# Kernel tuning notes

Hardware: AMD Instinct MI355X
Metric: run time of the kernel (lower is better)

The kernel has to match this reference:

```python
import jax, jax.numpy as jnp
import numpy as np

HIDDEN = 64
LATENT = 32
HEADS = 4
EDGE_DIM = 3
NEG_SLOPE = 0.2
N_NODES = 50000
N_EDGES = 400000
IN_DIM = 128
NUM_CLASSES = 10
NUM_GRAPHS = 64


def _gatv2_layer(x, src, dst, edge_attr, Wl, Wr, We, att, b):
    # x: [N, F]; src/dst: [E] (self-loops already included); edge_attr: [E, 3]
    N = x.shape[0]
    xl = (x @ Wl).reshape(N, HEADS, HIDDEN)          # source transform (lin_l)
    xr = (x @ Wr).reshape(N, HEADS, HIDDEN)          # target transform (lin_r)
    e = (edge_attr @ We).reshape(-1, HEADS, HIDDEN)  # edge transform (lin_edge)
    s = jax.nn.leaky_relu(xl[src] + xr[dst] + e, NEG_SLOPE)   # [E,H,C]
    logits = jnp.einsum('ehc,hc->eh', s, att)                 # [E,H]
    # segment softmax over incoming edges of each destination node
    m = jax.ops.segment_max(logits, dst, num_segments=N)      # [N,H]
    ex = jnp.exp(logits - m[dst])
    denom = jax.ops.segment_sum(ex, dst, num_segments=N)      # [N,H]
    alpha = ex / denom[dst]                                   # [E,H]
    msg = xl[src] * alpha[:, :, None]                         # [E,H,C]
    out = jax.ops.segment_sum(msg, dst, num_segments=N)       # [N,H,C]
    return out.mean(axis=1) + b                               # concat=False -> head mean


def setup_inputs() -> dict:
    key = jax.random.key(0)
    ks = jax.random.split(key, 24)
    inp = {}
    inp['x'] = jax.random.normal(ks[0], (N_NODES, IN_DIM), dtype=jnp.float32)
    inp['edge_index'] = jax.random.randint(ks[1], (2, N_EDGES), 0, N_NODES)
    inp['edge_attr'] = jax.random.normal(ks[2], (N_EDGES, EDGE_DIM), dtype=jnp.float32)
    inp['batch'] = jnp.sort(jax.random.randint(ks[3], (N_NODES,), 0, NUM_GRAPHS))
    HC = HEADS * HIDDEN

    def glorot(k, shape):
        fan = shape[0] + shape[-1]
        return jax.random.normal(k, shape, dtype=jnp.float32) * jnp.sqrt(2.0 / fan)

    # layer 0 (in_dim -> hidden), layer 1 (hidden -> hidden)
    inp['Wl0'] = glorot(ks[4], (IN_DIM, HC)); inp['Wr0'] = glorot(ks[5], (IN_DIM, HC))
    inp['We0'] = glorot(ks[6], (EDGE_DIM, HC)); inp['att0'] = glorot(ks[7], (HEADS, HIDDEN))
    inp['b0'] = jnp.zeros((HIDDEN,), jnp.float32)
    inp['Wl1'] = glorot(ks[8], (HIDDEN, HC)); inp['Wr1'] = glorot(ks[9], (HIDDEN, HC))
    inp['We1'] = glorot(ks[10], (EDGE_DIM, HC)); inp['att1'] = glorot(ks[11], (HEADS, HIDDEN))
    inp['b1'] = jnp.zeros((HIDDEN,), jnp.float32)
    inp['W_mu'] = glorot(ks[12], (HIDDEN, LATENT)); inp['b_mu'] = jnp.zeros((LATENT,), jnp.float32)
    inp['W_dec'] = glorot(ks[13], (LATENT, IN_DIM)); inp['b_dec'] = jnp.zeros((IN_DIM,), jnp.float32)
    inp['W_cls'] = glorot(ks[14], (LATENT, NUM_CLASSES)); inp['b_cls'] = jnp.zeros((NUM_CLASSES,), jnp.float32)
    inp['weight'] = jax.random.normal(ks[15], (LATENT,), dtype=jnp.float32)
    return inp


def reference(x, edge_index, edge_attr, batch,
              Wl0, Wr0, We0, att0, b0,
              Wl1, Wr1, We1, att1, b1,
              W_mu, b_mu, W_dec, b_dec, W_cls, b_cls, weight):
    N = x.shape[0]
    # add self-loops once (PyG add_self_loops=True; edge_attr fill_value='mean')
    loops = jnp.arange(N, dtype=edge_index.dtype)
    src = jnp.concatenate([edge_index[0], loops])
    dst = jnp.concatenate([edge_index[1], loops])
    ea_mean = jnp.mean(edge_attr, axis=0)
    ea = jnp.concatenate([edge_attr, jnp.broadcast_to(ea_mean, (N, EDGE_DIM))], axis=0)

    h = jax.nn.relu(_gatv2_layer(x, src, dst, ea, Wl0, Wr0, We0, att0, b0))
    h = jax.nn.relu(_gatv2_layer(h, src, dst, ea, Wl1, Wr1, We1, att1, b1))
    z = h @ W_mu + b_mu                                   # [N, LATENT]

    recon = z @ W_dec + b_dec                             # node_recon: [N, in_dim]
    link = jnp.sum(z[edge_index[0]] * z[edge_index[1]] * weight, axis=1)  # [E]
    g_emb = jax.ops.segment_sum(z, batch, num_segments=NUM_GRAPHS)        # global_add_pool
    logits = g_emb @ W_cls + b_cls                        # [G, num_classes]
    return z, recon, link, logits
```

## Files before the change

kernel.cpp:

```cpp
#include <hip/hip_runtime.h>
#include <math.h>

#define HIDDEN 64
#define LATENT 32
#define HEADS 4
#define IN_DIM 128
#define NUM_CLASSES 10
#define NUM_GRAPHS 64
#define NEG_SLOPE 0.2f
#define HC 256

__global__ void k_easum(const float* __restrict__ ea, int E, float* __restrict__ ea_sum) {
    float s0 = 0.f, s1 = 0.f, s2 = 0.f;
    for (int e = blockIdx.x * blockDim.x + threadIdx.x; e < E; e += gridDim.x * blockDim.x) {
        s0 += ea[e * 3 + 0];
        s1 += ea[e * 3 + 1];
        s2 += ea[e * 3 + 2];
    }
    for (int off = 32; off; off >>= 1) {
        s0 += __shfl_xor(s0, off);
        s1 += __shfl_xor(s1, off);
        s2 += __shfl_xor(s2, off);
    }
    if ((threadIdx.x & 63) == 0) {
        atomicAdd(&ea_sum[0], s0);
        atomicAdd(&ea_sum[1], s1);
        atomicAdd(&ea_sum[2], s2);
    }
}

__global__ void k_hist(const int* __restrict__ ei, int* __restrict__ deg, int E0) {
    int e = blockIdx.x * blockDim.x + threadIdx.x;
    if (e < E0) atomicAdd(&deg[ei[E0 + e]], 1);
}

__global__ void k_scan1(const int* __restrict__ deg, int* __restrict__ off,
                        int* __restrict__ bsum, int N) {
    __shared__ int sh[256];
    int t = threadIdx.x, i = blockIdx.x * 256 + t;
    int v = (i < N) ? deg[i] : 0;
    sh[t] = v;
    __syncthreads();
    for (int d = 1; d < 256; d <<= 1) {
        int x = (t >= d) ? sh[t - d] : 0;
        __syncthreads();
        sh[t] += x;
        __syncthreads();
    }
    if (i < N) off[i] = sh[t] - v;
    if (t == 255) bsum[blockIdx.x] = sh[255];
}

__global__ void k_scan2(int* __restrict__ bsum, int nb) {
    __shared__ int sh[256];
    int t = threadIdx.x;
    int v = (t < nb) ? bsum[t] : 0;
    sh[t] = v;
    __syncthreads();
    for (int d = 1; d < 256; d <<= 1) {
        int x = (t >= d) ? sh[t - d] : 0;
        __syncthreads();
        sh[t] += x;
        __syncthreads();
    }
    if (t < nb) bsum[t] = sh[t] - v;
}

__global__ void k_scan3(int* __restrict__ off, const int* __restrict__ bsum,
                        int* __restrict__ cur, int N) {
    int i = blockIdx.x * 256 + threadIdx.x;
    if (i >= N) return;
    int o = off[i] + bsum[blockIdx.x];
    off[i] = o;
    cur[i] = o;
}

__global__ void k_scatter(const int* __restrict__ ei, const float* __restrict__ ea,
                          int* __restrict__ cur, int* __restrict__ csr_src,
                          float4* __restrict__ csr_a, int E0) {
    int e = blockIdx.x * blockDim.x + threadIdx.x;
    if (e >= E0) return;
    int dst = ei[E0 + e];
    int pos = atomicAdd(&cur[dst], 1);
    csr_src[pos] = ei[e];
    csr_a[pos] = make_float4(ea[e * 3], ea[e * 3 + 1], ea[e * 3 + 2], 0.f);
}

template <int K, int NPB>
__global__ void k_dual_gemm(const float* __restrict__ X, const float* __restrict__ Wl,
                            const float* __restrict__ Wr, float* __restrict__ xl,
                            float* __restrict__ xr, int N) {
    __shared__ float sx[NPB][K];
    int node0 = blockIdx.x * NPB;
    int tid = threadIdx.x;
    for (int i = tid; i < NPB * K; i += blockDim.x) {
        int n = i / K, k = i % K;
        int gn = node0 + n;
        sx[n][k] = (gn < N) ? X[(long)gn * K + k] : 0.f;
    }
    __syncthreads();
    int col = tid;
    float accl[NPB], accr[NPB];
#pragma unroll
    for (int n = 0; n < NPB; n++) { accl[n] = 0.f; accr[n] = 0.f; }
    for (int k = 0; k < K; k++) {
        float wl = Wl[k * HC + col];
        float wr = Wr[k * HC + col];
#pragma unroll
        for (int n = 0; n < NPB; n++) {
            accl[n] += sx[n][k] * wl;
            accr[n] += sx[n][k] * wr;
        }
    }
#pragma unroll
    for (int n = 0; n < NPB; n++) {
        int gn = node0 + n;
        if (gn < N) {
            xl[(long)gn * HC + col] = accl[n];
            xr[(long)gn * HC + col] = accr[n];
        }
    }
}

__global__ void k_gat(const float* __restrict__ xl, const float* __restrict__ xr,
                      const int* __restrict__ csr_src, const float4* __restrict__ csr_a,
                      const int* __restrict__ off, const int* __restrict__ deg,
                      const float* __restrict__ easum, float invE,
                      const float* __restrict__ We, const float* __restrict__ att,
                      const float* __restrict__ bias, float* __restrict__ out, int N) {
    int wid = (blockIdx.x * blockDim.x + threadIdx.x) >> 6;
    int L = threadIdx.x & 63;
    if (wid >= N) return;
    int n = wid;

    float4 xr4 = ((const float4*)(xr + (size_t)n * HC))[L];
    float4 w0 = ((const float4*)We)[L];
    float4 w1 = ((const float4*)(We + HC))[L];
    float4 w2 = ((const float4*)(We + 2 * HC))[L];
    float4 at = ((const float4*)att)[L];
    float am0 = easum[0] * invE, am1 = easum[1] * invE, am2 = easum[2] * invE;

    float m = -INFINITY, d = 0.f;
    float acc0 = 0.f, acc1 = 0.f, acc2 = 0.f, acc3 = 0.f;
    int base = off[n], cnt = deg[n];

    for (int i = -1; i < cnt; i++) {
        int src;
        float a0, a1, a2;
        if (i < 0) {
            src = n;
            a0 = am0; a1 = am1; a2 = am2;
        } else {
            src = csr_src[base + i];
            float4 a = csr_a[base + i];
            a0 = a.x; a1 = a.y; a2 = a.z;
        }
        float4 xs = ((const float4*)(xl + (size_t)src * HC))[L];
        float s0 = xs.x + xr4.x + (a0 * w0.x + a1 * w1.x + a2 * w2.x);
        float s1 = xs.y + xr4.y + (a0 * w0.y + a1 * w1.y + a2 * w2.y);
        float s2 = xs.z + xr4.z + (a0 * w0.z + a1 * w1.z + a2 * w2.z);
        float s3 = xs.w + xr4.w + (a0 * w0.w + a1 * w1.w + a2 * w2.w);
        s0 = (s0 > 0.f) ? s0 : NEG_SLOPE * s0;
        s1 = (s1 > 0.f) ? s1 : NEG_SLOPE * s1;
        s2 = (s2 > 0.f) ? s2 : NEG_SLOPE * s2;
        s3 = (s3 > 0.f) ? s3 : NEG_SLOPE * s3;
        float p = s0 * at.x + s1 * at.y + s2 * at.z + s3 * at.w;
        p += __shfl_xor(p, 1);
        p += __shfl_xor(p, 2);
        p += __shfl_xor(p, 4);
        p += __shfl_xor(p, 8);
        float mn = fmaxf(m, p);
        float sc = __expf(m - mn);
        float ex = __expf(p - mn);
        d = d * sc + ex;
        acc0 = acc0 * sc + ex * xs.x;
        acc1 = acc1 * sc + ex * xs.y;
        acc2 = acc2 * sc + ex * xs.z;
        acc3 = acc3 * sc + ex * xs.w;
        m = mn;
    }
    float inv_d = 1.f / d;
    float v0 = acc0 * inv_d, v1 = acc1 * inv_d, v2 = acc2 * inv_d, v3 = acc3 * inv_d;
    v0 += __shfl_xor(v0, 16); v1 += __shfl_xor(v1, 16);
    v2 += __shfl_xor(v2, 16); v3 += __shfl_xor(v3, 16);
    v0 += __shfl_xor(v0, 32); v1 += __shfl_xor(v1, 32);
    v2 += __shfl_xor(v2, 32); v3 += __shfl_xor(v3, 32);
    if (L < 16) {
        float4 bx = ((const float4*)bias)[L];
        float4 o;
        o.x = fmaxf(0.25f * v0 + bx.x, 0.f);
        o.y = fmaxf(0.25f * v1 + bx.y, 0.f);
        o.z = fmaxf(0.25f * v2 + bx.z, 0.f);
        o.w = fmaxf(0.25f * v3 + bx.w, 0.f);
        ((float4*)(out + (size_t)n * HIDDEN))[L] = o;
    }
}

__global__ void k_mu(const float* __restrict__ h, const float* __restrict__ Wmu,
                     const float* __restrict__ bmu, float* __restrict__ z, int N) {
    int i = blockIdx.x * blockDim.x + threadIdx.x;
    if (i >= N * LATENT) return;
    int n = i >> 5, j = i & 31;
    const float* hr = h + (long)n * 64;
    float acc = bmu[j];
#pragma unroll
    for (int k = 0; k < 64; k++) acc += hr[k] * Wmu[k * LATENT + j];
    z[i] = acc;
}

__global__ void k_dec(const float* __restrict__ z, const float* __restrict__ W,
                      const float* __restrict__ b, float* __restrict__ out, int N) {
    int i = blockIdx.x * blockDim.x + threadIdx.x;
    if (i >= N * IN_DIM) return;
    int n = i >> 7, j = i & 127;
    const float* zr = z + (long)n * LATENT;
    float acc = b[j];
#pragma unroll
    for (int k = 0; k < LATENT; k++) acc += zr[k] * W[k * IN_DIM + j];
    out[i] = acc;
}

__global__ void k_link(const float* __restrict__ z, const int* __restrict__ ei,
                       const float* __restrict__ w, float* __restrict__ link, int E0) {
    int t = blockIdx.x * blockDim.x + threadIdx.x;
    int e = t >> 5;
    int c = t & 31;
    if (e >= E0) return;
    int s = ei[e], d = ei[E0 + e];
    float v = z[(long)s * LATENT + c] * z[(long)d * LATENT + c] * w[c];
    for (int off = 16; off; off >>= 1) v += __shfl_xor(v, off);
    if (c == 0) link[e] = v;
}

__global__ void k_pool(const float* __restrict__ z, const int* __restrict__ batch,
                       float* __restrict__ gemb, int N) {
    int i = blockIdx.x * blockDim.x + threadIdx.x;
    if (i >= N * LATENT) return;
    int n = i >> 5, j = i & 31;
    atomicAdd(&gemb[batch[n] * LATENT + j], z[i]);
}

__global__ void k_cls(const float* __restrict__ g, const float* __restrict__ W,
                      const float* __restrict__ b, float* __restrict__ out) {
    int i = blockIdx.x * blockDim.x + threadIdx.x;
    if (i >= NUM_GRAPHS * NUM_CLASSES) return;
    int gi = i / NUM_CLASSES, j = i % NUM_CLASSES;
    float acc = b[j];
#pragma unroll
    for (int k = 0; k < LATENT; k++) acc += g[gi * LATENT + k] * W[k * NUM_CLASSES + j];
    out[i] = acc;
}

extern "C" void kernel_launch(void* const* d_in, const int* in_sizes, int n_in, void* d_out,
                              int out_size, void* d_ws, size_t ws_size, hipStream_t stream) {
    const float* x = (const float*)d_in[0];
    const int* ei = (const int*)d_in[1];
    const float* ea = (const float*)d_in[2];
    const int* batch = (const int*)d_in[3];
    const float* Wl0 = (const float*)d_in[4];
    const float* Wr0 = (const float*)d_in[5];
    const float* We0 = (const float*)d_in[6];
    const float* att0 = (const float*)d_in[7];
    const float* b0 = (const float*)d_in[8];
    const float* Wl1 = (const float*)d_in[9];
    const float* Wr1 = (const float*)d_in[10];
    const float* We1 = (const float*)d_in[11];
    const float* att1 = (const float*)d_in[12];
    const float* b1 = (const float*)d_in[13];
    const float* Wmu = (const float*)d_in[14];
    const float* bmu = (const float*)d_in[15];
    const float* Wdec = (const float*)d_in[16];
    const float* bdec = (const float*)d_in[17];
    const float* Wcls = (const float*)d_in[18];
    const float* bcls = (const float*)d_in[19];
    const float* weight = (const float*)d_in[20];

    const int N = in_sizes[0] / IN_DIM;
    const int E0 = in_sizes[1] / 2;

    float* ws = (float*)d_ws;
    size_t o = 0;
    float* A = ws + o; o += (size_t)N * HC;
    float* B = ws + o; o += (size_t)N * HC;
    float4* csr_a = (float4*)(ws + o); o += (size_t)E0 * 4;
    int* csr_src = (int*)(ws + o); o += E0;
    int* deg = (int*)(ws + o); o += N;
    int* coff = (int*)(ws + o); o += N;
    int* cur = (int*)(ws + o); o += N;
    int* bsum = (int*)(ws + o); o += 256;
    float* G = ws + o; o += (size_t)N * HIDDEN;
    float* easum = ws + o; o += 16;
    float* gemb = ws + o; o += NUM_GRAPHS * LATENT;

    float* out = (float*)d_out;
    float* z_out = out;
    float* recon_out = out + (size_t)N * LATENT;
    float* link_out = recon_out + (size_t)N * IN_DIM;
    float* logits_out = link_out + (size_t)E0;

    const int TB = 256;
    const int nb = (N + 255) / 256;
    const int nodeBlocks = (N * 64 + TB - 1) / TB;
    const float invE = 1.f / (float)E0;

    hipMemsetAsync(deg, 0, (size_t)N * sizeof(int), stream);
    hipMemsetAsync(easum, 0, 16 * sizeof(float), stream);
    hipMemsetAsync(gemb, 0, NUM_GRAPHS * LATENT * sizeof(float), stream);
    k_easum<<<256, TB, 0, stream>>>(ea, E0, easum);
    k_hist<<<(E0 + TB - 1) / TB, TB, 0, stream>>>(ei, deg, E0);
    k_scan1<<<nb, 256, 0, stream>>>(deg, coff, bsum, N);
    k_scan2<<<1, 256, 0, stream>>>(bsum, nb);
    k_scan3<<<nb, 256, 0, stream>>>(coff, bsum, cur, N);
    k_scatter<<<(E0 + TB - 1) / TB, TB, 0, stream>>>(ei, ea, cur, csr_src, csr_a, E0);

    k_dual_gemm<IN_DIM, 8><<<(N + 7) / 8, TB, 0, stream>>>(x, Wl0, Wr0, A, B, N);
    k_gat<<<nodeBlocks, TB, 0, stream>>>(A, B, csr_src, csr_a, coff, deg, easum, invE, We0,
                                         att0, b0, G, N);

    k_dual_gemm<HIDDEN, 8><<<(N + 7) / 8, TB, 0, stream>>>(G, Wl1, Wr1, A, B, N);
    k_gat<<<nodeBlocks, TB, 0, stream>>>(A, B, csr_src, csr_a, coff, deg, easum, invE, We1,
                                         att1, b1, G, N);

    k_mu<<<(N * LATENT + TB - 1) / TB, TB, 0, stream>>>(G, Wmu, bmu, z_out, N);
    k_dec<<<(N * IN_DIM + TB - 1) / TB, TB, 0, stream>>>(z_out, Wdec, bdec, recon_out, N);
    k_link<<<(E0 * 32 + TB - 1) / TB, TB, 0, stream>>>(z_out, ei, weight, link_out, E0);
    k_pool<<<(N * LATENT + TB - 1) / TB, TB, 0, stream>>>(z_out, batch, gemb, N);
    k_cls<<<(NUM_GRAPHS * NUM_CLASSES + TB - 1) / TB, TB, 0, stream>>>(gemb, Wcls, bcls,
                                                                       logits_out);
}
```

Before: 763.2 us.

## Replace dual node GEMM with 128x128 register-tiled SGEMM kernel

```diff
diff --git a/kernel.cpp b/kernel.cpp
--- a/kernel.cpp
+++ b/kernel.cpp
@@ -86,38 +86,73 @@
     csr_a[pos] = make_float4(ea[e * 3], ea[e * 3 + 1], ea[e * 3 + 2], 0.f);
 }
 
-template <int K, int NPB>
-__global__ void k_dual_gemm(const float* __restrict__ X, const float* __restrict__ Wl,
-                            const float* __restrict__ Wr, float* __restrict__ xl,
-                            float* __restrict__ xr, int N) {
-    __shared__ float sx[NPB][K];
-    int node0 = blockIdx.x * NPB;
-    int tid = threadIdx.x;
-    for (int i = tid; i < NPB * K; i += blockDim.x) {
-        int n = i / K, k = i % K;
-        int gn = node0 + n;
-        sx[n][k] = (gn < N) ? X[(long)gn * K + k] : 0.f;
-    }
-    __syncthreads();
-    int col = tid;
-    float accl[NPB], accr[NPB];
-#pragma unroll
-    for (int n = 0; n < NPB; n++) { accl[n] = 0.f; accr[n] = 0.f; }
-    for (int k = 0; k < K; k++) {
-        float wl = Wl[k * HC + col];
-        float wr = Wr[k * HC + col];
-#pragma unroll
-        for (int n = 0; n < NPB; n++) {
-            accl[n] += sx[n][k] * wl;
-            accr[n] += sx[n][k] * wr;
+template <int K>
+__global__ __launch_bounds__(256, 2) void k_gemm(const float* __restrict__ X,
+                                                 const float* __restrict__ Wl,
+                                                 const float* __restrict__ Wr,
+                                                 float* __restrict__ xl, float* __restrict__ xr,
+                                                 int N) {
+    constexpr int KC = 64;
+    constexpr int PAD = 132;
+    __shared__ float sx[KC * PAD];
+
+    const int M0 = blockIdx.x * 128;
+    const int nt = blockIdx.y;
+    const float* W = ((nt < 2) ? Wl : Wr) + (nt & 1) * 128;
+    float* out = ((nt < 2) ? xl : xr) + (nt & 1) * 128;
+
+    const int t = threadIdx.x;
+    const int tr = t >> 4;
+    const int tc = t & 15;
+
+    float acc[8][8];
+#pragma unroll
+    for (int i = 0; i < 8; i++)
+#pragma unroll
+        for (int j = 0; j < 8; j++) acc[i][j] = 0.f;
+
+    const int kq = t & 15;
+    const int nsub = t >> 4;
+
+    for (int kc0 = 0; kc0 < K; kc0 += KC) {
+        __syncthreads();
+#pragma unroll
+        for (int pass = 0; pass < 8; ++pass) {
+            int node = pass * 16 + nsub;
+            int gn = M0 + node;
+            float4 v = make_float4(0.f, 0.f, 0.f, 0.f);
+            if (gn < N) v = ((const float4*)(X + (size_t)gn * K + kc0))[kq];
+            int k = kq * 4;
+            sx[(k + 0) * PAD + node] = v.x;
+            sx[(k + 1) * PAD + node] = v.y;
+            sx[(k + 2) * PAD + node] = v.z;
+            sx[(k + 3) * PAD + node] = v.w;
         }
-    }
-#pragma unroll
-    for (int n = 0; n < NPB; n++) {
-        int gn = node0 + n;
+        __syncthreads();
+
+        const float* Wc = W + (size_t)kc0 * HC;
+#pragma unroll 4
+        for (int k = 0; k < KC; ++k) {
+            float4 a0 = *(const float4*)&sx[k * PAD + tr * 8];
+            float4 a1 = *(const float4*)&sx[k * PAD + tr * 8 + 4];
+            float4 b0 = *(const float4*)&Wc[(size_t)k * HC + tc * 8];
+            float4 b1 = *(const float4*)&Wc[(size_t)k * HC + tc * 8 + 4];
+            float a[8] = {a0.x, a0.y, a0.z, a0.w, a1.x, a1.y, a1.z, a1.w};
+            float b[8] = {b0.x, b0.y, b0.z, b0.w, b1.x, b1.y, b1.z, b1.w};
+#pragma unroll
+            for (int i = 0; i < 8; i++)
+#pragma unroll
+                for (int j = 0; j < 8; j++) acc[i][j] += a[i] * b[j];
+        }
+    }
+
+#pragma unroll
+    for (int i = 0; i < 8; i++) {
+        int gn = M0 + tr * 8 + i;
         if (gn < N) {
-            xl[(long)gn * HC + col] = accl[n];
-            xr[(long)gn * HC + col] = accr[n];
+            float* p = out + (size_t)gn * HC + tc * 8;
+            ((float4*)p)[0] = make_float4(acc[i][0], acc[i][1], acc[i][2], acc[i][3]);
+            ((float4*)p)[1] = make_float4(acc[i][4], acc[i][5], acc[i][6], acc[i][7]);
         }
     }
 }
@@ -302,6 +337,7 @@
     const int nb = (N + 255) / 256;
     const int nodeBlocks = (N * 64 + TB - 1) / TB;
     const float invE = 1.f / (float)E0;
+    const dim3 gemmGrid((N + 127) / 128, 4);
 
     hipMemsetAsync(deg, 0, (size_t)N * sizeof(int), stream);
     hipMemsetAsync(easum, 0, 16 * sizeof(float), stream);
@@ -313,11 +349,11 @@
     k_scan3<<<nb, 256, 0, stream>>>(coff, bsum, cur, N);
     k_scatter<<<(E0 + TB - 1) / TB, TB, 0, stream>>>(ei, ea, cur, csr_src, csr_a, E0);
 
-    k_dual_gemm<IN_DIM, 8><<<(N + 7) / 8, TB, 0, stream>>>(x, Wl0, Wr0, A, B, N);
+    k_gemm<IN_DIM><<<gemmGrid, TB, 0, stream>>>(x, Wl0, Wr0, A, B, N);
     k_gat<<<nodeBlocks, TB, 0, stream>>>(A, B, csr_src, csr_a, coff, deg, easum, invE, We0,
                                          att0, b0, G, N);
 
-    k_dual_gemm<HIDDEN, 8><<<(N + 7) / 8, TB, 0, stream>>>(G, Wl1, Wr1, A, B, N);
+    k_gemm<HIDDEN><<<gemmGrid, TB, 0, stream>>>(G, Wl1, Wr1, A, B, N);
     k_gat<<<nodeBlocks, TB, 0, stream>>>(A, B, csr_src, csr_a, coff, deg, easum, invE, We1,
                                          att1, b1, G, N);
 
```

After: 752.0 us. No clear change (-1.5%).

## Rewrite dual GEMM with 16-node tiles and transposed vectorized shared-memory loads

Applied to the files above, without the earlier changes.

```diff
diff --git a/kernel.cpp b/kernel.cpp
--- a/kernel.cpp
+++ b/kernel.cpp
@@ -86,38 +86,60 @@
     csr_a[pos] = make_float4(ea[e * 3], ea[e * 3 + 1], ea[e * 3 + 2], 0.f);
 }
 
-template <int K, int NPB>
-__global__ void k_dual_gemm(const float* __restrict__ X, const float* __restrict__ Wl,
-                            const float* __restrict__ Wr, float* __restrict__ xl,
-                            float* __restrict__ xr, int N) {
-    __shared__ float sx[NPB][K];
-    int node0 = blockIdx.x * NPB;
-    int tid = threadIdx.x;
-    for (int i = tid; i < NPB * K; i += blockDim.x) {
-        int n = i / K, k = i % K;
-        int gn = node0 + n;
-        sx[n][k] = (gn < N) ? X[(long)gn * K + k] : 0.f;
+template <int K>
+__global__ void k_gemm(const float* __restrict__ X, const float* __restrict__ Wl,
+                       const float* __restrict__ Wr, float* __restrict__ xl,
+                       float* __restrict__ xr, int N) {
+    constexpr int NPB = 16;
+    constexpr int LDR = 20;
+    __shared__ float sxt[K * LDR];
+
+    const int t = threadIdx.x;
+    const int M0 = blockIdx.x * NPB;
+
+    constexpr int NV4 = NPB * K / 4;
+#pragma unroll
+    for (int idx = t; idx < NV4; idx += 256) {
+        int node = idx & 15;
+        int kq = idx >> 4;
+        float4 v = make_float4(0.f, 0.f, 0.f, 0.f);
+        if (M0 + node < N) v = ((const float4*)(X + (size_t)(M0 + node) * K))[kq];
+        int k = kq * 4;
+        sxt[(k + 0) * LDR + node] = v.x;
+        sxt[(k + 1) * LDR + node] = v.y;
+        sxt[(k + 2) * LDR + node] = v.z;
+        sxt[(k + 3) * LDR + node] = v.w;
     }
     __syncthreads();
-    int col = tid;
+
     float accl[NPB], accr[NPB];
 #pragma unroll
     for (int n = 0; n < NPB; n++) { accl[n] = 0.f; accr[n] = 0.f; }
+
+    const float* wlp = Wl + t;
+    const float* wrp = Wr + t;
+#pragma unroll 4
     for (int k = 0; k < K; k++) {
-        float wl = Wl[k * HC + col];
-        float wr = Wr[k * HC + col];
+        float wl = wlp[(size_t)k * HC];
+        float wr = wrp[(size_t)k * HC];
+        float a[NPB];
+        *(float4*)&a[0] = *(const float4*)&sxt[k * LDR + 0];
+        *(float4*)&a[4] = *(const float4*)&sxt[k * LDR + 4];
+        *(float4*)&a[8] = *(const float4*)&sxt[k * LDR + 8];
+        *(float4*)&a[12] = *(const float4*)&sxt[k * LDR + 12];
 #pragma unroll
         for (int n = 0; n < NPB; n++) {
-            accl[n] += sx[n][k] * wl;
-            accr[n] += sx[n][k] * wr;
+            accl[n] += a[n] * wl;
+            accr[n] += a[n] * wr;
         }
     }
+
 #pragma unroll
     for (int n = 0; n < NPB; n++) {
-        int gn = node0 + n;
+        int gn = M0 + n;
         if (gn < N) {
-            xl[(long)gn * HC + col] = accl[n];
-            xr[(long)gn * HC + col] = accr[n];
+            xl[(size_t)gn * HC + t] = accl[n];
+            xr[(size_t)gn * HC + t] = accr[n];
         }
     }
 }
@@ -138,7 +160,6 @@
     float4 w1 = ((const float4*)(We + HC))[L];
     float4 w2 = ((const float4*)(We + 2 * HC))[L];
     float4 at = ((const float4*)att)[L];
-    float am0 = easum[0] * invE, am1 = easum[1] * invE, am2 = easum[2] * invE;
 
     float m = -INFINITY, d = 0.f;
     float acc0 = 0.f, acc1 = 0.f, acc2 = 0.f, acc3 = 0.f;
@@ -149,7 +170,9 @@
         float a0, a1, a2;
         if (i < 0) {
             src = n;
-            a0 = am0; a1 = am1; a2 = am2;
+            a0 = easum[0] * invE;
+            a1 = easum[1] * invE;
+            a2 = easum[2] * invE;
         } else {
             src = csr_src[base + i];
             float4 a = csr_a[base + i];
@@ -302,6 +325,7 @@
     const int nb = (N + 255) / 256;
     const int nodeBlocks = (N * 64 + TB - 1) / TB;
     const float invE = 1.f / (float)E0;
+    const int gemmBlocks = (N + 15) / 16;
 
     hipMemsetAsync(deg, 0, (size_t)N * sizeof(int), stream);
     hipMemsetAsync(easum, 0, 16 * sizeof(float), stream);
@@ -313,11 +337,11 @@
     k_scan3<<<nb, 256, 0, stream>>>(coff, bsum, cur, N);
     k_scatter<<<(E0 + TB - 1) / TB, TB, 0, stream>>>(ei, ea, cur, csr_src, csr_a, E0);
 
-    k_dual_gemm<IN_DIM, 8><<<(N + 7) / 8, TB, 0, stream>>>(x, Wl0, Wr0, A, B, N);
+    k_gemm<IN_DIM><<<gemmBlocks, TB, 0, stream>>>(x, Wl0, Wr0, A, B, N);
     k_gat<<<nodeBlocks, TB, 0, stream>>>(A, B, csr_src, csr_a, coff, deg, easum, invE, We0,
                                          att0, b0, G, N);
 
-    k_dual_gemm<HIDDEN, 8><<<(N + 7) / 8, TB, 0, stream>>>(G, Wl1, Wr1, A, B, N);
+    k_gemm<HIDDEN><<<gemmBlocks, TB, 0, stream>>>(G, Wl1, Wr1, A, B, N);
     k_gat<<<nodeBlocks, TB, 0, stream>>>(A, B, csr_src, csr_a, coff, deg, easum, invE, We1,
                                          att1, b1, G, N);
 
```

New measurement: 713.2 us. -6.6%, faster.
